# Optimization experiments

Measured on AMD Instinct MI355X. Metric: run time of the kernel, lower is better.

Reference implementation:

```python
import jax, jax.numpy as jnp
import numpy as np

F_DIM = 128        # feature_dim
LATENT = 256       # latent_dim
HEADS = 4          # n_head
N_GRAPHS = 256
NODES_PER = 100    # < 180 (pos table size)
N = N_GRAPHS * NODES_PER
DEG = 8
E = N * DEG
MAX_POS = 180
NEG_SLOPE = 0.2


def sinusoid_table(n_node, d):
    pos = np.arange(n_node, dtype=np.float64)[:, None]
    j = np.arange(d, dtype=np.float64)[None, :]
    ang = pos / np.power(10000.0, 2.0 * (np.floor(j / 2.0)) / d)
    ang[:, 0::2] = np.sin(ang[:, 0::2])
    ang[:, 1::2] = np.cos(ang[:, 1::2])
    return jnp.asarray(ang, dtype=jnp.float32)  # [n_node, d]


def gat_layer(x, src, dst, W, a_src, a_dst, bias):
    # x: [N, in], W: [in, H*C], a_src/a_dst: [H, C], bias: [H*C]
    H, C = a_src.shape
    xl = (x @ W).reshape(N, H, C)                      # [N,H,C]
    s = jnp.einsum('nhc,hc->nh', xl, a_src)            # [N,H]
    d = jnp.einsum('nhc,hc->nh', xl, a_dst)            # [N,H]
    e = jax.nn.leaky_relu(s[src] + d[dst], NEG_SLOPE)  # [E,H]
    emax = jax.ops.segment_max(e, dst, num_segments=N)
    ex = jnp.exp(e - emax[dst])
    den = jax.ops.segment_sum(ex, dst, num_segments=N)
    alpha = ex / (den[dst] + 1e-16)                    # [E,H]
    out = jax.ops.segment_sum(alpha[:, :, None] * xl[src], dst, num_segments=N)
    return out.reshape(N, H * C) + bias


def setup_inputs() -> dict:
    key = jax.random.key(0)
    ks = jax.random.split(key, 20)
    sc = 0.05
    z = jax.random.normal(ks[0], (N_GRAPHS, LATENT), dtype=jnp.float32)
    batch = jnp.repeat(jnp.arange(N_GRAPHS, dtype=jnp.int64), NODES_PER)
    base = (jnp.arange(N, dtype=jnp.int64) // NODES_PER) * NODES_PER
    nbr = jax.random.randint(ks[1], (N, DEG), 0, NODES_PER, dtype=jnp.int64)
    src = (base[:, None] + nbr).reshape(-1)
    dst = jnp.repeat(jnp.arange(N, dtype=jnp.int64), DEG)
    edge_index = jnp.stack([src, dst], 0)
    HF = HEADS * F_DIM
    p = {
        'W0': jax.random.normal(ks[2], (LATENT, F_DIM)) * sc,
        'b0': jnp.zeros((F_DIM,), jnp.float32),
        'W1': jax.random.normal(ks[3], (2 * F_DIM, HF)) * sc,
        'as1': jax.random.normal(ks[4], (HEADS, F_DIM)) * sc,
        'ad1': jax.random.normal(ks[5], (HEADS, F_DIM)) * sc,
        'b1': jnp.zeros((HF,), jnp.float32),
        'W2': jax.random.normal(ks[6], (HF, HF)) * sc,
        'as2': jax.random.normal(ks[7], (HEADS, F_DIM)) * sc,
        'ad2': jax.random.normal(ks[8], (HEADS, F_DIM)) * sc,
        'b2': jnp.zeros((HF,), jnp.float32),
        'W3': jax.random.normal(ks[9], (HF, HF)) * sc,
        'as3': jax.random.normal(ks[10], (HEADS, F_DIM)) * sc,
        'ad3': jax.random.normal(ks[11], (HEADS, F_DIM)) * sc,
        'b3': jnp.zeros((HF,), jnp.float32),
        'Wg': jax.random.normal(ks[12], (HF, F_DIM)) * sc,
        'bg': jnp.zeros((F_DIM,), jnp.float32),
        'Wf': jax.random.normal(ks[13], (F_DIM, 5)) * sc,
        'bf': jnp.zeros((5,), jnp.float32),
    }
    return {'z': z, 'edge_index': edge_index, 'batch': batch, **p}


def reference(z, edge_index, batch, W0, b0, W1, as1, ad1, b1,
              W2, as2, ad2, b2, W3, as3, ad3, b3, Wg, bg, Wf, bf):
    # node order within each graph (intended semantics of node_order_within_batch)
    counts = jax.ops.segment_sum(jnp.ones((N,), jnp.int32), batch, num_segments=N_GRAPHS)
    cum = jnp.concatenate([jnp.zeros((1,), jnp.int32), jnp.cumsum(counts)[:-1]])
    order = jnp.arange(N, dtype=jnp.int32) - cum[batch]
    pos = sinusoid_table(MAX_POS, F_DIM)[order]        # [N, F]  (detached buffer)

    h = (z @ W0 + b0)[batch]                           # [N, F]
    h = jax.nn.relu(jnp.concatenate([h, pos], axis=1)) # [N, 2F]

    # PyG GATConv default add_self_loops=True
    loop = jnp.arange(N, dtype=edge_index.dtype)
    src = jnp.concatenate([edge_index[0], loop])
    dst = jnp.concatenate([edge_index[1], loop])

    h = jax.nn.relu(gat_layer(h, src, dst, W1, as1, ad1, b1))
    h = jax.nn.relu(gat_layer(h, src, dst, W2, as2, ad2, b2))
    h = jax.nn.relu(gat_layer(h, src, dst, W3, as3, ad3, b3))
    h = jax.nn.relu(h @ Wg + bg)
    return h @ Wf + bf                                 # [N, 5]
```

## Files before the change

kernel.cpp:

```cpp
#include <hip/hip_runtime.h>
#include <hip/hip_bf16.h>
#include <math.h>

#define N_GRAPHS 256
#define NODES_PER 100
#define NN (N_GRAPHS * NODES_PER)
#define DEG 8
#define FD 128
#define LAT 256
#define HFD 512
#define MAXPOS 180
#define NEG_SLOPE 0.2f

typedef _Float16 half8 __attribute__((ext_vector_type(8)));
typedef float float4v __attribute__((ext_vector_type(4)));

__device__ __forceinline__ int xcd_swz(int bid, int total) {
    int q = total >> 3;
    return (bid & 7) * q + (bid >> 3);
}

__global__ void sintab_kernel(float* __restrict__ tab) {
    int p = blockIdx.x;
    int j = threadIdx.x;
    double ang = (double)p / pow(10000.0, (double)(2 * (j / 2)) / 128.0);
    double v = (j & 1) ? cos(ang) : sin(ang);
    tab[p * FD + j] = (float)v;
}

__global__ void g0_kernel(const float* __restrict__ z, const float* __restrict__ W0,
                          const float* __restrict__ b0, float* __restrict__ g0) {
    __shared__ float s_z[LAT];
    int g = blockIdx.x;
    int j = threadIdx.x;
    s_z[j]       = z[g * LAT + j];
    s_z[j + 128] = z[g * LAT + 128 + j];
    __syncthreads();
    float acc = 0.f;
    #pragma unroll 8
    for (int k = 0; k < LAT; ++k)
        acc += s_z[k] * W0[k * FD + j];
    g0[g * FD + j] = acc + b0[j];
}

__global__ void build_x1_kernel(const float* __restrict__ g0, const float* __restrict__ tab,
                                const int* __restrict__ batch, _Float16* __restrict__ x1) {
    __shared__ int s_b, s_ord;
    int i = blockIdx.x;
    int t = threadIdx.x;
    if (t == 0) {
        int b = batch[i];
        int lo = 0, hi = i;
        while (lo < hi) { int mid = (lo + hi) >> 1; if (batch[mid] < b) lo = mid + 1; else hi = mid; }
        s_b = b;
        s_ord = i - lo;
    }
    __syncthreads();
    float v = (t < 128) ? g0[s_b * FD + t] : tab[s_ord * FD + (t - 128)];
    x1[(size_t)i * 256 + t] = (_Float16)fmaxf(v, 0.f);
}

__global__ void wconv_all_kernel(const float* __restrict__ W1, const float* __restrict__ W2,
                                 const float* __restrict__ W3, const float* __restrict__ Wg,
                                 _Float16* __restrict__ W1t, _Float16* __restrict__ W2t,
                                 _Float16* __restrict__ W3t, _Float16* __restrict__ Wgt) {
    __shared__ float tile[32][33];
    int b = blockIdx.x;
    const float* in; _Float16* out; int K, Nw, tid2;
    if (b < 128)      { in = W1; out = W1t; K = 256; Nw = 512; tid2 = b; }
    else if (b < 384) { in = W2; out = W2t; K = 512; Nw = 512; tid2 = b - 128; }
    else if (b < 640) { in = W3; out = W3t; K = 512; Nw = 512; tid2 = b - 384; }
    else              { in = Wg; out = Wgt; K = 512; Nw = 128; tid2 = b - 640; }
    int nxt = Nw / 32;
    int nb = (tid2 % nxt) * 32, kb = (tid2 / nxt) * 32;
    int tx = threadIdx.x & 31, ty = threadIdx.x >> 5;
    #pragma unroll
    for (int r = 0; r < 4; ++r)
        tile[ty + 8 * r][tx] = in[(size_t)(kb + ty + 8 * r) * Nw + nb + tx];
    __syncthreads();
    #pragma unroll
    for (int r = 0; r < 4; ++r)
        out[(size_t)(nb + ty + 8 * r) * K + kb + tx] = (_Float16)tile[tx][ty + 8 * r];
}

template <int MODE>
__global__ __launch_bounds__(256) void hgemm_kernel(
    const _Float16* __restrict__ X,
    const _Float16* __restrict__ Wt,
    const float* __restrict__ bias,
    const float* __restrict__ a_src,
    const float* __restrict__ a_dst,
    float* __restrict__ sbuf,
    float* __restrict__ dbuf,
    const float* __restrict__ Wf,
    const float* __restrict__ bfv,
    void* __restrict__ Yv,
    int K, int ldy, int nbx) {
    __shared__ __align__(16) _Float16 As[2][128 * 32];
    __shared__ __align__(16) _Float16 Bs[2][128 * 32];
    __shared__ float red[5][128][2];
    const int lin = xcd_swz(blockIdx.x, gridDim.x);
    const int row0 = (lin / nbx) * 128;
    const int col0 = (lin % nbx) * 128;
    const int tid  = threadIdx.x;
    const int lane = tid & 63;
    const int wave = tid >> 6;
    const int wm = wave >> 1;
    const int wn = wave & 1;

    const int sr = tid >> 1;
    const int sq = (tid & 1) * 2;
    const size_t ga = (size_t)(row0 + sr) * K + sq * 8;
    const size_t gb = (size_t)(col0 + sr) * K + sq * 8;
    const int ss = (sr >> 1) & 3;
    const int w0 = sr * 32 + ((sq ^ ss) * 8);
    const int w1 = sr * 32 + (((sq + 1) ^ ss) * 8);

    const int kq  = lane >> 4;
    const int l15 = lane & 15;

    float4v acc[4][4];
    #pragma unroll
    for (int i = 0; i < 4; ++i)
        #pragma unroll
        for (int j = 0; j < 4; ++j)
            acc[i][j] = (float4v){0.f, 0.f, 0.f, 0.f};

    half8 ra0, ra1, rb0, rb1;
    ra0 = *(const half8*)&X[ga];      ra1 = *(const half8*)&X[ga + 8];
    rb0 = *(const half8*)&Wt[gb];     rb1 = *(const half8*)&Wt[gb + 8];
    *(half8*)&As[0][w0] = ra0;  *(half8*)&As[0][w1] = ra1;
    *(half8*)&Bs[0][w0] = rb0;  *(half8*)&Bs[0][w1] = rb1;

    const int nk = K >> 5;
    for (int ks = 0; ks < nk; ++ks) {
        __syncthreads();
        const int cur = ks & 1;
        if (ks + 1 < nk) {
            int kb = (ks + 1) << 5;
            ra0 = *(const half8*)&X[ga + kb];   ra1 = *(const half8*)&X[ga + kb + 8];
            rb0 = *(const half8*)&Wt[gb + kb];  rb1 = *(const half8*)&Wt[gb + kb + 8];
        }
        half8 af[4], bf[4];
        #pragma unroll
        for (int mi = 0; mi < 4; ++mi) {
            int r = wm * 64 + mi * 16 + l15;
            af[mi] = *(const half8*)&As[cur][r * 32 + ((kq ^ ((r >> 1) & 3)) * 8)];
        }
        #pragma unroll
        for (int ni = 0; ni < 4; ++ni) {
            int c = wn * 64 + ni * 16 + l15;
            bf[ni] = *(const half8*)&Bs[cur][c * 32 + ((kq ^ ((c >> 1) & 3)) * 8)];
        }
        #pragma unroll
        for (int mi = 0; mi < 4; ++mi)
            #pragma unroll
            for (int ni = 0; ni < 4; ++ni)
                acc[mi][ni] = __builtin_amdgcn_mfma_f32_16x16x32_f16(af[mi], bf[ni], acc[mi][ni], 0, 0, 0);
        if (ks + 1 < nk) {
            const int nxt2 = cur ^ 1;
            *(half8*)&As[nxt2][w0] = ra0;  *(half8*)&As[nxt2][w1] = ra1;
            *(half8*)&Bs[nxt2][w0] = rb0;  *(half8*)&Bs[nxt2][w1] = rb1;
        }
    }

    if (MODE == 0) {
        const int h = col0 >> 7;
        float asv[4], adv[4];
        #pragma unroll
        for (int ni = 0; ni < 4; ++ni) {
            int ch = wn * 64 + ni * 16 + l15;
            asv[ni] = a_src[h * FD + ch];
            adv[ni] = a_dst[h * FD + ch];
        }
        #pragma unroll
        for (int mi = 0; mi < 4; ++mi) {
            int rb = row0 + wm * 64 + mi * 16 + ((lane >> 4) << 2);
            #pragma unroll
            for (int j = 0; j < 4; ++j) {
                float ps = 0.f, pd = 0.f;
                #pragma unroll
                for (int ni = 0; ni < 4; ++ni) {
                    float v = acc[mi][ni][j];
                    int c = col0 + wn * 64 + ni * 16 + l15;
                    ((_Float16*)Yv)[(size_t)(rb + j) * ldy + c] = (_Float16)v;
                    ps += v * asv[ni];
                    pd += v * adv[ni];
                }
                #pragma unroll
                for (int m = 8; m >= 1; m >>= 1) {
                    ps += __shfl_xor(ps, m);
                    pd += __shfl_xor(pd, m);
                }
                if (l15 == 0) {
                    int rloc = wm * 64 + mi * 16 + ((lane >> 4) << 2) + j;
                    red[0][rloc][wn] = ps;
                    red[1][rloc][wn] = pd;
                }
            }
        }
        __syncthreads();
        if (tid < 128) {
            sbuf[(size_t)(row0 + tid) * 4 + h] = red[0][tid][0] + red[0][tid][1];
            dbuf[(size_t)(row0 + tid) * 4 + h] = red[1][tid][0] + red[1][tid][1];
        }
    } else {
        float bgv[4], wf[4][5];
        #pragma unroll
        for (int ni = 0; ni < 4; ++ni) {
            int c = wn * 64 + ni * 16 + l15;
            bgv[ni] = bias[c];
            #pragma unroll
            for (int q = 0; q < 5; ++q) wf[ni][q] = Wf[c * 5 + q];
        }
        #pragma unroll
        for (int mi = 0; mi < 4; ++mi) {
            #pragma unroll
            for (int j = 0; j < 4; ++j) {
                float vr[4];
                #pragma unroll
                for (int ni = 0; ni < 4; ++ni)
                    vr[ni] = fmaxf(acc[mi][ni][j] + bgv[ni], 0.f);
                #pragma unroll
                for (int q = 0; q < 5; ++q) {
                    float p = vr[0] * wf[0][q] + vr[1] * wf[1][q] + vr[2] * wf[2][q] + vr[3] * wf[3][q];
                    #pragma unroll
                    for (int m = 8; m >= 1; m >>= 1) p += __shfl_xor(p, m);
                    if (l15 == 0) {
                        int rloc = wm * 64 + mi * 16 + ((lane >> 4) << 2) + j;
                        red[q][rloc][wn] = p;
                    }
                }
            }
        }
        __syncthreads();
        if (tid < 128) {
            float* o = (float*)Yv;
            #pragma unroll
            for (int q = 0; q < 5; ++q)
                o[(size_t)(row0 + tid) * 5 + q] = red[q][tid][0] + red[q][tid][1] + bfv[q];
        }
    }
}

__global__ void agg_kernel(const _Float16* __restrict__ xl,
                           const float* __restrict__ s, const float* __restrict__ d,
                           const int* __restrict__ esrc,
                           const float* __restrict__ bias,
                           _Float16* __restrict__ xout) {
    int wave = threadIdx.x >> 6;
    int lane = threadIdx.x & 63;
    int blk = xcd_swz(blockIdx.x, gridDim.x);
    int i = blk * 4 + wave;
    int h = lane >> 4;

    int sk = (lane < 8) ? esrc[i * DEG + lane] : i;
    int srcs[9];
    #pragma unroll
    for (int k = 0; k < 9; ++k) srcs[k] = __shfl(sk, k);

    float dh = d[i * 4 + h];
    float e[9];
    float m = -1e30f;
    #pragma unroll
    for (int k = 0; k < 9; ++k) {
        float v = s[srcs[k] * 4 + h] + dh;
        v = (v >= 0.f) ? v : NEG_SLOPE * v;
        e[k] = v;
        m = fmaxf(m, v);
    }
    float den = 0.f;
    #pragma unroll
    for (int k = 0; k < 9; ++k) { e[k] = __expf(e[k] - m); den += e[k]; }
    float inv = 1.f / (den + 1e-16f);

    int c0 = lane * 8;
    float acc[8] = {};
    #pragma unroll
    for (int k = 0; k < 9; ++k) {
        half8 x = *(const half8*)&xl[(size_t)srcs[k] * HFD + c0];
        float a = e[k] * inv;
        #pragma unroll
        for (int j = 0; j < 8; ++j) acc[j] += a * (float)x[j];
    }
    float4v b0 = *(const float4v*)&bias[c0];
    float4v b1 = *(const float4v*)&bias[c0 + 4];
    half8 o;
    #pragma unroll
    for (int j = 0; j < 4; ++j) {
        o[j]     = (_Float16)fmaxf(acc[j] + b0[j], 0.f);
        o[j + 4] = (_Float16)fmaxf(acc[j + 4] + b1[j], 0.f);
    }
    *(half8*)&xout[(size_t)i * HFD + c0] = o;
}

extern "C" void kernel_launch(void* const* d_in, const int* in_sizes, int n_in,
                              void* d_out, int out_size, void* d_ws, size_t ws_size,
                              hipStream_t stream) {
    const float* z    = (const float*)d_in[0];
    const int*  eidx  = (const int*)d_in[1];
    const int*  batch = (const int*)d_in[2];
    const float* W0  = (const float*)d_in[3];
    const float* b0  = (const float*)d_in[4];
    const float* W1  = (const float*)d_in[5];
    const float* as1 = (const float*)d_in[6];
    const float* ad1 = (const float*)d_in[7];
    const float* b1  = (const float*)d_in[8];
    const float* W2  = (const float*)d_in[9];
    const float* as2 = (const float*)d_in[10];
    const float* ad2 = (const float*)d_in[11];
    const float* b2  = (const float*)d_in[12];
    const float* W3  = (const float*)d_in[13];
    const float* as3 = (const float*)d_in[14];
    const float* ad3 = (const float*)d_in[15];
    const float* b3  = (const float*)d_in[16];
    const float* Wg  = (const float*)d_in[17];
    const float* bg  = (const float*)d_in[18];
    const float* Wf  = (const float*)d_in[19];
    const float* bfv = (const float*)d_in[20];
    float* out = (float*)d_out;

    float* ws   = (float*)d_ws;
    float* tab  = ws;
    float* g0   = tab + 23040;
    float* sbuf = g0 + 32768;
    float* dbuf = sbuf + (size_t)NN * 4;
    _Float16* Yh  = (_Float16*)(dbuf + (size_t)NN * 4);
    _Float16* Xh  = Yh + (size_t)NN * 512;
    _Float16* W1t = Xh + (size_t)NN * 512;
    _Float16* W2t = W1t + 512 * 256;
    _Float16* W3t = W2t + 512 * 512;
    _Float16* Wgt = W3t + 512 * 512;

    sintab_kernel<<<MAXPOS, FD, 0, stream>>>(tab);
    g0_kernel<<<N_GRAPHS, FD, 0, stream>>>(z, W0, b0, g0);
    build_x1_kernel<<<NN, 256, 0, stream>>>(g0, tab, batch, Xh);
    wconv_all_kernel<<<704, 256, 0, stream>>>(W1, W2, W3, Wg, W1t, W2t, W3t, Wgt);

    const int nbL = (NN / 128) * (HFD / 128);
    const int nbH = (NN / 128) * (FD / 128);

    hgemm_kernel<0><<<nbL, 256, 0, stream>>>(Xh, W1t, nullptr, as1, ad1, sbuf, dbuf, nullptr, nullptr, Yh, 256, HFD, HFD / 128);
    agg_kernel<<<NN / 4, 256, 0, stream>>>(Yh, sbuf, dbuf, eidx, b1, Xh);

    hgemm_kernel<0><<<nbL, 256, 0, stream>>>(Xh, W2t, nullptr, as2, ad2, sbuf, dbuf, nullptr, nullptr, Yh, 512, HFD, HFD / 128);
    agg_kernel<<<NN / 4, 256, 0, stream>>>(Yh, sbuf, dbuf, eidx, b2, Xh);

    hgemm_kernel<0><<<nbL, 256, 0, stream>>>(Xh, W3t, nullptr, as3, ad3, sbuf, dbuf, nullptr, nullptr, Yh, 512, HFD, HFD / 128);
    agg_kernel<<<NN / 4, 256, 0, stream>>>(Yh, sbuf, dbuf, eidx, b3, Xh);

    hgemm_kernel<1><<<nbH, 256, 0, stream>>>(Xh, Wgt, bg, nullptr, nullptr, nullptr, nullptr, Wf, bfv, out, 512, 5, FD / 128);
}
```

Measured before the change: 294.3 us.

## Use direct global-to-LDS loads in GEMM and compute sinusoids inline

```diff
diff --git a/kernel.cpp b/kernel.cpp
--- a/kernel.cpp
+++ b/kernel.cpp
@@ -9,7 +9,6 @@
 #define FD 128
 #define LAT 256
 #define HFD 512
-#define MAXPOS 180
 #define NEG_SLOPE 0.2f
 
 typedef _Float16 half8 __attribute__((ext_vector_type(8)));
@@ -20,12 +19,10 @@
     return (bid & 7) * q + (bid >> 3);
 }
 
-__global__ void sintab_kernel(float* __restrict__ tab) {
-    int p = blockIdx.x;
-    int j = threadIdx.x;
-    double ang = (double)p / pow(10000.0, (double)(2 * (j / 2)) / 128.0);
-    double v = (j & 1) ? cos(ang) : sin(ang);
-    tab[p * FD + j] = (float)v;
+__device__ __forceinline__ void gload_lds16(const _Float16* g, _Float16* l) {
+    __builtin_amdgcn_global_load_lds(
+        (const __attribute__((address_space(1))) unsigned int*)g,
+        (__attribute__((address_space(3))) unsigned int*)l, 16, 0, 0);
 }
 
 __global__ void g0_kernel(const float* __restrict__ z, const float* __restrict__ W0,
@@ -43,7 +40,7 @@
     g0[g * FD + j] = acc + b0[j];
 }
 
-__global__ void build_x1_kernel(const float* __restrict__ g0, const float* __restrict__ tab,
+__global__ void build_x1_kernel(const float* __restrict__ g0,
                                 const int* __restrict__ batch, _Float16* __restrict__ x1) {
     __shared__ int s_b, s_ord;
     int i = blockIdx.x;
@@ -56,7 +53,16 @@
         s_ord = i - lo;
     }
     __syncthreads();
-    float v = (t < 128) ? g0[s_b * FD + t] : tab[s_ord * FD + (t - 128)];
+    float v;
+    if (t < 128) {
+        v = g0[s_b * FD + t];
+    } else {
+        int j = t - 128;
+        int j2 = j >> 1;
+        float freq = expf(-(float)j2 * 0.1439115683f);
+        float ang = (float)s_ord * freq;
+        v = (j & 1) ? cosf(ang) : sinf(ang);
+    }
     x1[(size_t)i * 256 + t] = (_Float16)fmaxf(v, 0.f);
 }
 
@@ -96,8 +102,8 @@
     const float* __restrict__ bfv,
     void* __restrict__ Yv,
     int K, int ldy, int nbx) {
-    __shared__ __align__(16) _Float16 As[2][128 * 32];
-    __shared__ __align__(16) _Float16 Bs[2][128 * 32];
+    __shared__ __align__(16) _Float16 As[128 * 32];
+    __shared__ __align__(16) _Float16 Bs[128 * 32];
     __shared__ float red[5][128][2];
     const int lin = xcd_swz(blockIdx.x, gridDim.x);
     const int row0 = (lin / nbx) * 128;
@@ -108,13 +114,16 @@
     const int wm = wave >> 1;
     const int wn = wave & 1;
 
-    const int sr = tid >> 1;
-    const int sq = (tid & 1) * 2;
-    const size_t ga = (size_t)(row0 + sr) * K + sq * 8;
-    const size_t gb = (size_t)(col0 + sr) * K + sq * 8;
-    const int ss = (sr >> 1) & 3;
-    const int w0 = sr * 32 + ((sq ^ ss) * 8);
-    const int w1 = sr * 32 + (((sq + 1) ^ ss) * 8);
+    const int srow = tid >> 2;
+    const int sq   = (tid & 3) ^ ((tid >> 3) & 3);
+    const _Float16* gA0 = X  + (size_t)(row0 + srow) * K + sq * 8;
+    const _Float16* gB0 = Wt + (size_t)(col0 + srow) * K + sq * 8;
+    const _Float16* gA1 = gA0 + (size_t)64 * K;
+    const _Float16* gB1 = gB0 + (size_t)64 * K;
+    _Float16* ldsA0 = &As[wave * 512];
+    _Float16* ldsA1 = &As[2048 + wave * 512];
+    _Float16* ldsB0 = &Bs[wave * 512];
+    _Float16* ldsB1 = &Bs[2048 + wave * 512];
 
     const int kq  = lane >> 4;
     const int l15 = lane & 15;
@@ -126,42 +135,30 @@
         for (int j = 0; j < 4; ++j)
             acc[i][j] = (float4v){0.f, 0.f, 0.f, 0.f};
 
-    half8 ra0, ra1, rb0, rb1;
-    ra0 = *(const half8*)&X[ga];      ra1 = *(const half8*)&X[ga + 8];
-    rb0 = *(const half8*)&Wt[gb];     rb1 = *(const half8*)&Wt[gb + 8];
-    *(half8*)&As[0][w0] = ra0;  *(half8*)&As[0][w1] = ra1;
-    *(half8*)&Bs[0][w0] = rb0;  *(half8*)&Bs[0][w1] = rb1;
-
     const int nk = K >> 5;
     for (int ks = 0; ks < nk; ++ks) {
+        gload_lds16(gA0 + ks * 32, ldsA0);
+        gload_lds16(gA1 + ks * 32, ldsA1);
+        gload_lds16(gB0 + ks * 32, ldsB0);
+        gload_lds16(gB1 + ks * 32, ldsB1);
         __syncthreads();
-        const int cur = ks & 1;
-        if (ks + 1 < nk) {
-            int kb = (ks + 1) << 5;
-            ra0 = *(const half8*)&X[ga + kb];   ra1 = *(const half8*)&X[ga + kb + 8];
-            rb0 = *(const half8*)&Wt[gb + kb];  rb1 = *(const half8*)&Wt[gb + kb + 8];
-        }
-        half8 af[4], bf[4];
+        half8 af[4], bfr[4];
         #pragma unroll
         for (int mi = 0; mi < 4; ++mi) {
             int r = wm * 64 + mi * 16 + l15;
-            af[mi] = *(const half8*)&As[cur][r * 32 + ((kq ^ ((r >> 1) & 3)) * 8)];
+            af[mi] = *(const half8*)&As[r * 32 + ((kq ^ ((r >> 1) & 3)) * 8)];
         }
         #pragma unroll
         for (int ni = 0; ni < 4; ++ni) {
             int c = wn * 64 + ni * 16 + l15;
-            bf[ni] = *(const half8*)&Bs[cur][c * 32 + ((kq ^ ((c >> 1) & 3)) * 8)];
+            bfr[ni] = *(const half8*)&Bs[c * 32 + ((kq ^ ((c >> 1) & 3)) * 8)];
         }
         #pragma unroll
         for (int mi = 0; mi < 4; ++mi)
             #pragma unroll
             for (int ni = 0; ni < 4; ++ni)
-                acc[mi][ni] = __builtin_amdgcn_mfma_f32_16x16x32_f16(af[mi], bf[ni], acc[mi][ni], 0, 0, 0);
-        if (ks + 1 < nk) {
-            const int nxt2 = cur ^ 1;
-            *(half8*)&As[nxt2][w0] = ra0;  *(half8*)&As[nxt2][w1] = ra1;
-            *(half8*)&Bs[nxt2][w0] = rb0;  *(half8*)&Bs[nxt2][w1] = rb1;
-        }
+                acc[mi][ni] = __builtin_amdgcn_mfma_f32_16x16x32_f16(af[mi], bfr[ni], acc[mi][ni], 0, 0, 0);
+        __syncthreads();
     }
 
     if (MODE == 0) {
@@ -321,8 +318,7 @@
     float* out = (float*)d_out;
 
     float* ws   = (float*)d_ws;
-    float* tab  = ws;
-    float* g0   = tab + 23040;
+    float* g0   = ws;
     float* sbuf = g0 + 32768;
     float* dbuf = sbuf + (size_t)NN * 4;
     _Float16* Yh  = (_Float16*)(dbuf + (size_t)NN * 4);
@@ -332,9 +328,8 @@
     _Float16* W3t = W2t + 512 * 512;
     _Float16* Wgt = W3t + 512 * 512;
 
-    sintab_kernel<<<MAXPOS, FD, 0, stream>>>(tab);
     g0_kernel<<<N_GRAPHS, FD, 0, stream>>>(z, W0, b0, g0);
-    build_x1_kernel<<<NN, 256, 0, stream>>>(g0, tab, batch, Xh);
+    build_x1_kernel<<<NN, 256, 0, stream>>>(g0, batch, Xh);
     wconv_all_kernel<<<704, 256, 0, stream>>>(W1, W2, W3, Wg, W1t, W2t, W3t, Wgt);
 
     const int nbL = (NN / 128) * (HFD / 128);
```

Measured after the change: 306.9 us. +4.3%, slower.
